# Kernel optimization log

Measured on AMD Instinct MI355X. Metric: run time of the kernel, lower is better.

Reference implementation:

```python
import jax, jax.numpy as jnp
import numpy as np
from jax import lax

B, L = 16384, 32
HID, CIN = 8, 2
N_SUB = 2            # RK4 substeps per spline interval (fixed-step stand-in for torchcde's adaptive solver)
T10_LO, T10_HI = 0.1, 7.0


def push_zeros(a):
    # torch: move nonzero entries of each row to the right end, zeros to the left.
    # stable ascending sort on validity key (0 for zeros, 1 for valid) reproduces this exactly
    # because the invalid entries are exactly 0.
    keys = (a != 0).astype(jnp.int32)
    order = jnp.argsort(keys, axis=1)  # jax sorts are stable
    return jnp.take_along_axis(a, order, axis=1)


def setup_inputs() -> dict:
    key = jax.random.key(0)
    ks = jax.random.split(key, 12)
    fa_len = jax.random.randint(ks[0], (B, 1), L // 2, L + 1)          # 16..32 valid points
    valid = jnp.arange(L)[None, :] < fa_len                             # (B, L)
    X_fa_in = jnp.where(valid, jax.random.uniform(ks[1], (B, L), minval=0.1, maxval=1.1), 0.0)
    fa_vals_in = jnp.where(valid, jax.random.uniform(ks[2], (B, L), minval=0.05, maxval=0.45), 0.0)
    TR_vals = jax.random.uniform(ks[3], (B, 1), minval=0.003, maxval=0.01)
    fa_mask = valid

    def lin(k, fout, fin):
        kw, kb = jax.random.split(k)
        s = 1.0 / np.sqrt(fin)
        return (jax.random.uniform(kw, (fout, fin), minval=-s, maxval=s),
                jax.random.uniform(kb, (fout,), minval=-s, maxval=s))

    W_init, b_init = lin(ks[4], HID, CIN)        # self.initial: Linear(2, 8)
    W1, b1 = lin(ks[5], 256, HID)                # CDE_Func.linear1
    W2, b2 = lin(ks[6], CIN * HID, 256)          # CDE_Func.linear2
    Wr1, br1 = lin(ks[7], 200, HID)              # reg_T10
    Wr2, br2 = lin(ks[8], 200, 200)
    Wr3, br3 = lin(ks[9], 1, 200)
    return dict(X_fa_in=X_fa_in, fa_vals_in=fa_vals_in, TR_vals=TR_vals,
                W_init=W_init, b_init=b_init, W1=W1, b1=b1, W2=W2, b2=b2,
                Wr1=Wr1, br1=br1, Wr2=Wr2, br2=br2, Wr3=Wr3, br3=br3,
                fa_mask=fa_mask, fa_len=fa_len)


def _forward(X_fa_in, fa_vals_in, TR_vals, W_init, b_init, W1, b1, W2, b2,
             Wr1, br1, Wr2, br2, Wr3, br3, fa_mask, fa_len):
    fl = fa_len[:, 0]                       # (B,) int
    fl_f = fl.astype(X_fa_in.dtype)
    mean = jnp.sum(X_fa_in, axis=1) / fl_f
    Xn = X_fa_in / mean[:, None]
    X_fa = push_zeros(Xn)
    fa_vals = push_zeros(fa_vals_in)
    bidx = jnp.arange(X_fa.shape[0])
    last_X = X_fa[bidx, fl - 1][:, None]            # pushed array indexed at fa_len-1 (as in torch)
    last_fa = fa_vals_in[bidx, fl - 1][:, None]     # original array indexed at fa_len-1
    X_fa = jnp.where(X_fa == 0.0, last_X, X_fa)
    fa_vals = jnp.where(fa_vals == 0.0, last_fa, fa_vals)
    x = jnp.stack([fa_vals, X_fa], axis=-1)         # (B, L, 2): channels (fa, X)

    # Hermite cubic with backward differences, unit knot spacing t_i = i
    diffs = x[:, 1:] - x[:, :-1]                    # (B, L-1, C)
    m = jnp.concatenate([diffs[:, :1], diffs], axis=1)  # m_0 = fwd diff, m_i = backward diff
    X0s, X1s = x[:, :-1], x[:, 1:]                  # per-interval knot values (B, L-1, C)
    M0s, M1s = m[:, :-1], m[:, 1:]

    z0 = x[:, 0] @ W_init.T + b_init                # X.evaluate(interval[0]) == first knot

    def f(z):  # CDE vector field: (B, HID) -> (B, HID, CIN)
        h = jax.nn.relu(z @ W1.T + b1)
        g = jnp.tanh(h @ W2.T + b2)
        return g.reshape(z.shape[0], HID, CIN)

    hstep = 1.0 / N_SUB
    nI = x.shape[1] - 1
    intervals = jnp.repeat(jnp.arange(nI), N_SUB)
    s0s = jnp.tile(jnp.arange(N_SUB) * hstep, nI).astype(x.dtype)

    def step(z, ts):
        i, s0 = ts
        x0, x1 = X0s[:, i], X1s[:, i]
        m0, m1 = M0s[:, i], M1s[:, i]

        def dX(s):  # spline derivative dX/dt at local coord s in [0,1]
            s2 = s * s
            return ((6 * s2 - 6 * s) * x0 + (3 * s2 - 4 * s + 1) * m0 +
                    (-6 * s2 + 6 * s) * x1 + (3 * s2 - 2 * s) * m1)

        def F(s, zz):
            return jnp.einsum('bhc,bc->bh', f(zz), dX(s))

        k1 = F(s0, z)
        k2 = F(s0 + hstep / 2, z + 0.5 * hstep * k1)
        k3 = F(s0 + hstep / 2, z + 0.5 * hstep * k2)
        k4 = F(s0 + hstep, z + hstep * k3)
        return z + (hstep / 6) * (k1 + 2 * k2 + 2 * k3 + k4), None

    z_T, _ = lax.scan(step, z0, (intervals, s0s))

    h1 = jax.nn.gelu(z_T @ Wr1.T + br1, approximate=False)
    h2 = jax.nn.gelu(h1 @ Wr2.T + br2, approximate=False)
    t = (h2 @ Wr3.T + br3)[:, 0]
    T10 = T10_LO + jax.nn.sigmoid(t)[:, None] * (T10_HI - T10_LO)   # (B, 1)
    R1 = 1.0 / T10
    E = jnp.exp(-TR_vals * R1)                                      # (B, 1)
    X_out = (1 - E) * jnp.sin(fa_vals_in) / (1 - jnp.cos(fa_vals_in) * E)
    mean2 = jnp.sum(X_out, axis=1) / fl_f
    X_out = X_out / mean2[:, None]
    M0 = jnp.ones_like(T10)
    return X_out, T10, M0


def reference(X_fa_in, fa_vals_in, TR_vals, W_init, b_init, W1, b1, W2, b2,
              Wr1, br1, Wr2, br2, Wr3, br3, fa_mask, fa_len):
    return _forward(X_fa_in, fa_vals_in, TR_vals, W_init, b_init, W1, b1, W2, b2,
                    Wr1, br1, Wr2, br2, Wr3, br3, fa_mask, fa_len)
```

## Files before the change

### kernel.cpp

```cpp
#include <hip/hip_runtime.h>
#include <hip/hip_bf16.h>

#define B_ROWS 16384
#define L_SEQ  32

typedef _Float16 f16;
typedef __attribute__((ext_vector_type(8))) _Float16 f16x8;
typedef __attribute__((ext_vector_type(4))) float f32x4;
typedef __attribute__((ext_vector_type(4))) unsigned int u32x4;

__device__ __forceinline__ unsigned pkh(float a, float b) {
    return __builtin_bit_cast(unsigned, __builtin_amdgcn_cvt_pkrtz(a, b));
}
__device__ __forceinline__ float tanh_fast(float x) {
    float e = __expf(2.0f * x);
    float r = __builtin_amdgcn_rcpf(e + 1.0f);
    return fmaf(-2.0f, r, 1.0f);
}
__device__ __forceinline__ float gelu_exact(float x) {
    return 0.5f * x * (1.0f + erff(x * 0.70710678118654752440f));
}
__device__ __forceinline__ void pin4(u32x4& v) {
    unsigned x0 = v[0], x1 = v[1], x2 = v[2], x3 = v[3];
    asm volatile("" : "+v"(x0), "+v"(x1), "+v"(x2), "+v"(x3));
    v = (u32x4){x0, x1, x2, x3};
}

__global__ __launch_bounds__(256, 1) void ode_kernel(
    const float* __restrict__ Xin, const float* __restrict__ Fin,
    const int*   __restrict__ fa_len,
    const float* __restrict__ Wi,  const float* __restrict__ bi,
    const float* __restrict__ W1g, const float* __restrict__ b1g,
    const float* __restrict__ W2g, const float* __restrict__ b2g,
    float* __restrict__ zT)
{
    __shared__ __align__(16) float xm[64 * 132];
#define XM(r_, i_, c_) xm[(r_) * 132 + (i_) * 4 + (c_)]

    const int tid = threadIdx.x;
    const int g16 = tid >> 4, sub = tid & 15;

    float mean_r[4]; int fl_r[4];
#pragma unroll
    for (int r = 0; r < 4; ++r) {
        const int row_l = g16 * 4 + r;
        const int row   = blockIdx.x * 64 + row_l;
        const float* Xr = Xin + row * L_SEQ;
        const float* Fr = Fin + row * L_SEQ;
        float xr0 = Xr[sub], xr1 = Xr[sub + 16];
        float fr0 = Fr[sub], fr1 = Fr[sub + 16];
        fl_r[r] = fa_len[row];
        float s = xr0 + xr1;
        s += __shfl_xor(s, 1, 16);
        s += __shfl_xor(s, 2, 16);
        s += __shfl_xor(s, 4, 16);
        s += __shfl_xor(s, 8, 16);
        mean_r[r] = s / (float)fl_r[r];
        XM(row_l, sub, 0)      = fr0; XM(row_l, sub, 1)      = xr0;
        XM(row_l, sub + 16, 0) = fr1; XM(row_l, sub + 16, 1) = xr1;
    }
    __syncthreads();

    float ff[4][2], xf[4][2];
#pragma unroll
    for (int r = 0; r < 4; ++r) {
        const int row_l = g16 * 4 + r;
        const int fl = fl_r[r];
        const float mean = mean_r[r];
        const int shift = L_SEQ - fl;
        int lsrc  = fl - 1 - shift;
        int lsrcC = lsrc < 0 ? 0 : lsrc;
        float lastX = (lsrc >= 0) ? (XM(row_l, lsrcC, 1) / mean) : 0.0f;
        float lastF = XM(row_l, fl - 1, 0);
#pragma unroll
        for (int u = 0; u < 2; ++u) {
            int p = sub + u * 16;
            int src = p - shift;
            int sc  = src < 0 ? 0 : src;
            float fraw = XM(row_l, sc, 0);
            float xraw = XM(row_l, sc, 1);
            ff[r][u] = (src >= 0) ? fraw : lastF;
            xf[r][u] = (src >= 0) ? (xraw / mean) : lastX;
        }
    }
    __syncthreads();
#pragma unroll
    for (int r = 0; r < 4; ++r) {
        const int row_l = g16 * 4 + r;
#pragma unroll
        for (int u = 0; u < 2; ++u) {
            int p = sub + u * 16;
            XM(row_l, p, 0) = ff[r][u];
            XM(row_l, p, 1) = xf[r][u];
        }
    }
    __syncthreads();
#pragma unroll
    for (int r = 0; r < 4; ++r) {
        const int row_l = g16 * 4 + r;
#pragma unroll
        for (int u = 0; u < 2; ++u) {
            int p = sub + u * 16;
            int qd = (p == 0) ? 1 : p;
            XM(row_l, p, 2) = XM(row_l, qd, 0) - XM(row_l, qd - 1, 0);
            XM(row_l, p, 3) = XM(row_l, qd, 1) - XM(row_l, qd - 1, 1);
        }
    }
    __syncthreads();

    const int wv   = tid >> 6;
    const int lane = tid & 63;
    const int n    = lane & 15;
    const int q    = lane >> 4;
    const int rowl = wv * 16 + n;
    const int rowg = blockIdx.x * 64 + rowl;

    u32x4 a1[16];
#pragma unroll
    for (int t = 0; t < 16; ++t) {
        const float* wr = W1g + (t * 16 + n) * 8 + (q < 2 ? q * 4 : 0);
        float4 w4 = *(const float4*)wr;
        float b1v = b1g[t * 16 + n];
        unsigned d0 = (q < 2) ? pkh(w4.x, w4.y) : (q == 2 ? pkh(b1v, 0.0f) : 0u);
        unsigned d1 = (q < 2) ? pkh(w4.z, w4.w) : 0u;
        a1[t] = (u32x4){d0, d1, 0u, 0u};
        pin4(a1[t]);
    }
    u32x4 a2[8];
#pragma unroll
    for (int kk = 0; kk < 8; ++kk) {
        const float* w2r = W2g + n * 256 + kk * 32 + 4 * q;
        float4 p0 = *(const float4*)(w2r);
        float4 p1 = *(const float4*)(w2r + 16);
        a2[kk] = (u32x4){pkh(p0.x, p0.y), pkh(p0.z, p0.w), pkh(p1.x, p1.y), pkh(p1.z, p1.w)};
        pin4(a2[kk]);
    }
    f32x4 c2seed;
#pragma unroll
    for (int r = 0; r < 4; ++r) c2seed[r] = b2g[4 * q + r];

    float f0 = XM(rowl, 0, 0), X0 = XM(rowl, 0, 1);
    float z0 = fmaf(Wi[(2 * q) * 2], f0, fmaf(Wi[(2 * q) * 2 + 1], X0, bi[2 * q]));
    float z1 = fmaf(Wi[(2 * q + 1) * 2], f0, fmaf(Wi[(2 * q + 1) * 2 + 1], X0, bi[2 * q + 1]));

    const int bpi = (((q & 1) << 5) + n) << 2;
    const f32x4 zero4 = {0.f, 0.f, 0.f, 0.f};
    const f16x8 zf16 = {0, 0, 0, 0, 0, 0, 0, 0};

    auto FEVAL = [&](float zza, float zzb, float d0c, float d1c, float& ko0, float& ko1) {
        unsigned myz = pkh(zza, zzb);
        int b0 = __builtin_amdgcn_ds_bpermute(bpi, (int)myz);
        int b1 = __builtin_amdgcn_ds_bpermute(bpi + 64, (int)myz);
        unsigned bz0 = (q < 2) ? (unsigned)b0 : (q == 2 ? 0x3C00u : 0u);
        unsigned bz1 = (q < 2) ? (unsigned)b1 : 0u;
        f16x8 bz = __builtin_bit_cast(f16x8, (u32x4){bz0, bz1, 0u, 0u});

        f32x4 c1[16];
#pragma unroll
        for (int t = 0; t < 16; ++t)
            c1[t] = __builtin_amdgcn_mfma_f32_16x16x32_f16(
                __builtin_bit_cast(f16x8, a1[t]), bz, zero4, 0, 0, 0);

        f16x8 hf[8];
#pragma unroll
        for (int kk = 0; kk < 8; ++kk) {
            u32x4 w = (u32x4){pkh(c1[2 * kk][0],     c1[2 * kk][1]),
                              pkh(c1[2 * kk][2],     c1[2 * kk][3]),
                              pkh(c1[2 * kk + 1][0], c1[2 * kk + 1][1]),
                              pkh(c1[2 * kk + 1][2], c1[2 * kk + 1][3])};
            hf[kk] = __builtin_elementwise_max(__builtin_bit_cast(f16x8, w), zf16);
        }

        f32x4 c2a = c2seed, c2b = zero4;
#pragma unroll
        for (int kk = 0; kk < 4; ++kk) {
            c2a = __builtin_amdgcn_mfma_f32_16x16x32_f16(
                __builtin_bit_cast(f16x8, a2[kk]), hf[kk], c2a, 0, 0, 0);
            c2b = __builtin_amdgcn_mfma_f32_16x16x32_f16(
                __builtin_bit_cast(f16x8, a2[kk + 4]), hf[kk + 4], c2b, 0, 0, 0);
        }
        f32x4 G = c2a + c2b;

        float t0 = tanh_fast(G[0]), t1 = tanh_fast(G[1]);
        float t2 = tanh_fast(G[2]), t3 = tanh_fast(G[3]);
        ko0 = fmaf(t0, d0c, t1 * d1c);
        ko1 = fmaf(t2, d0c, t3 * d1c);
    };

#pragma unroll 1
    for (int i = 0; i < 31; ++i) {
        float4 P0 = *(const float4*)&XM(rowl, i, 0);
        float4 P1 = *(const float4*)&XM(rowl, i + 1, 0);
        float m0f = P0.z, m0X = P0.w, m1f = P1.z, m1X = P1.w;
        float df  = P0.x - P1.x, dXx = P0.y - P1.y;

        float d25f = fmaf(-1.125f, df,  fmaf(0.1875f, m0f, -0.3125f * m1f));
        float d25X = fmaf(-1.125f, dXx, fmaf(0.1875f, m0X, -0.3125f * m1X));
        float d50f = fmaf(-1.5f,   df,  fmaf(-0.25f,  m0f, -0.25f   * m1f));
        float d50X = fmaf(-1.5f,   dXx, fmaf(-0.25f,  m0X, -0.25f   * m1X));
        float d75f = fmaf(-1.125f, df,  fmaf(-0.3125f, m0f, 0.1875f * m1f));
        float d75X = fmaf(-1.125f, dXx, fmaf(-0.3125f, m0X, 0.1875f * m1X));

#pragma unroll 1
        for (int ssi = 0; ssi < 2; ++ssi) {
            float daf = ssi ? d50f : m0f,  daX = ssi ? d50X : m0X;
            float dbf = ssi ? d75f : d25f, dbX = ssi ? d75X : d25X;
            float ddf = ssi ? m1f  : d50f, ddX = ssi ? m1X  : d50X;

            float k1a, k1b, k2a, k2b, k3a, k3b, k4a, k4b, zza, zzb;
            FEVAL(z0, z1, daf, daX, k1a, k1b);
            zza = fmaf(0.25f, k1a, z0); zzb = fmaf(0.25f, k1b, z1);
            FEVAL(zza, zzb, dbf, dbX, k2a, k2b);
            zza = fmaf(0.25f, k2a, z0); zzb = fmaf(0.25f, k2b, z1);
            FEVAL(zza, zzb, dbf, dbX, k3a, k3b);
            zza = fmaf(0.5f, k3a, z0);  zzb = fmaf(0.5f, k3b, z1);
            FEVAL(zza, zzb, ddf, ddX, k4a, k4b);

            float ka = fmaf(2.f, k2a, k1a); ka = fmaf(2.f, k3a, ka);
            float kb = fmaf(2.f, k2b, k1b); kb = fmaf(2.f, k3b, kb);
            z0 = fmaf(1.f / 12.f, ka + k4a, z0);
            z1 = fmaf(1.f / 12.f, kb + k4b, z1);
        }
    }

    *(float2*)(zT + rowg * 8 + 2 * q) = make_float2(z0, z1);
#undef XM
}

__global__ __launch_bounds__(256, 1) void readout_kernel(
    const float* __restrict__ zT,
    const float* __restrict__ Fin,
    const float* __restrict__ TRv,
    const int*   __restrict__ fa_len,
    const float* __restrict__ Wr1, const float* __restrict__ br1,
    const float* __restrict__ Wr2, const float* __restrict__ br2,
    const float* __restrict__ Wr3, const float* __restrict__ br3,
    float* __restrict__ out)
{
    const int tid  = threadIdx.x;
    const int wv   = tid >> 6;
    const int lane = tid & 63;
    const int n    = lane & 15;
    const int q    = lane >> 4;
    const int rowg = blockIdx.x * 64 + wv * 16 + n;

    const f32x4 zero4 = {0.f, 0.f, 0.f, 0.f};

    u32x4 bzw = {0u, 0u, 0u, 0u};
    if (q < 2) {
        float4 z4 = *(const float4*)(zT + rowg * 8 + 4 * q);
        bzw[0] = pkh(z4.x, z4.y);
        bzw[1] = pkh(z4.z, z4.w);
    } else if (q == 2) {
        bzw[0] = 0x3C00u;
    }
    f16x8 bz = __builtin_bit_cast(f16x8, bzw);

    f32x4 c1[13];
#pragma unroll
    for (int t = 0; t < 13; ++t) {
        int m = 16 * t + n;
        u32x4 af = {0u, 0u, 0u, 0u};
        if (q < 2) {
            if (m < 200) {
                float4 w4 = *(const float4*)(Wr1 + m * 8 + 4 * q);
                af[0] = pkh(w4.x, w4.y);
                af[1] = pkh(w4.z, w4.w);
            }
        } else if (q == 2) {
            float b = (m < 200) ? br1[m] : 0.0f;
            af[0] = pkh(b, 0.0f);
        }
        c1[t] = __builtin_amdgcn_mfma_f32_16x16x32_f16(
            __builtin_bit_cast(f16x8, af), bz, zero4, 0, 0, 0);
    }

    f16x8 hf[7];
#pragma unroll
    for (int kk = 0; kk < 7; ++kk) {
        float g0 = gelu_exact(c1[2 * kk][0]), g1 = gelu_exact(c1[2 * kk][1]);
        float g2 = gelu_exact(c1[2 * kk][2]), g3 = gelu_exact(c1[2 * kk][3]);
        float g4 = 0.f, g5 = 0.f, g6 = 0.f, g7 = 0.f;
        if (kk < 6) {
            g4 = gelu_exact(c1[2 * kk + 1][0]); g5 = gelu_exact(c1[2 * kk + 1][1]);
            g6 = gelu_exact(c1[2 * kk + 1][2]); g7 = gelu_exact(c1[2 * kk + 1][3]);
        }
        u32x4 w = (u32x4){pkh(g0, g1), pkh(g2, g3), pkh(g4, g5), pkh(g6, g7)};
        hf[kk] = __builtin_bit_cast(f16x8, w);
    }

    float tpart = 0.0f;
#pragma unroll 1
    for (int mt = 0; mt < 13; ++mt) {
        int mb = 16 * mt + 4 * q;
        f32x4 c2 = zero4;
        if (mb + 3 < 200) c2 = *(const f32x4*)(br2 + mb);
        int m2 = 16 * mt + n;
#pragma unroll
        for (int kk = 0; kk < 7; ++kk) {
            u32x4 af = {0u, 0u, 0u, 0u};
            if (m2 < 200) {
                int k0 = 32 * kk + 4 * q;
                const float* wr = Wr2 + m2 * 200 + k0;
                if (k0 + 3 < 200) {
                    float4 wa = *(const float4*)(wr);
                    af[0] = pkh(wa.x, wa.y); af[1] = pkh(wa.z, wa.w);
                }
                if (k0 + 19 < 200) {
                    float4 wb = *(const float4*)(wr + 16);
                    af[2] = pkh(wb.x, wb.y); af[3] = pkh(wb.z, wb.w);
                }
            }
            c2 = __builtin_amdgcn_mfma_f32_16x16x32_f16(
                __builtin_bit_cast(f16x8, af), hf[kk], c2, 0, 0, 0);
        }
        float4 w3 = make_float4(0.f, 0.f, 0.f, 0.f);
        if (mb + 3 < 200) w3 = *(const float4*)(Wr3 + mb);
        tpart = fmaf(w3.x, gelu_exact(c2[0]), tpart);
        tpart = fmaf(w3.y, gelu_exact(c2[1]), tpart);
        tpart = fmaf(w3.z, gelu_exact(c2[2]), tpart);
        tpart = fmaf(w3.w, gelu_exact(c2[3]), tpart);
    }
    tpart += __shfl_xor(tpart, 16);
    tpart += __shfl_xor(tpart, 32);

    float tval = tpart + br3[0];
    float sig  = __fdividef(1.0f, 1.0f + __expf(-tval));
    float T10  = 0.1f + 6.9f * sig;
    float E    = __expf(-TRv[rowg] * __builtin_amdgcn_rcpf(T10));

    const float* Fr = Fin + rowg * 32 + 8 * q;
    float xo[8]; float ssum = 0.0f;
#pragma unroll
    for (int j = 0; j < 8; ++j) {
        float fa = Fr[j];
        float sn = __sinf(fa), cs = __cosf(fa);
        float v = __fdividef((1.0f - E) * sn, 1.0f - cs * E);
        xo[j] = v; ssum += v;
    }
    ssum += __shfl_xor(ssum, 16);
    ssum += __shfl_xor(ssum, 32);
    float mean2 = ssum / (float)fa_len[rowg];
    float inv   = __fdividef(1.0f, mean2);

    float4* dst = (float4*)(out + rowg * 32 + 8 * q);
    dst[0] = make_float4(xo[0] * inv, xo[1] * inv, xo[2] * inv, xo[3] * inv);
    dst[1] = make_float4(xo[4] * inv, xo[5] * inv, xo[6] * inv, xo[7] * inv);
    if (q == 0) {
        out[B_ROWS * L_SEQ + rowg] = T10;
        out[B_ROWS * L_SEQ + B_ROWS + rowg] = 1.0f;
    }
}

extern "C" void kernel_launch(void* const* d_in, const int* in_sizes, int n_in,
                              void* d_out, int out_size, void* d_ws, size_t ws_size,
                              hipStream_t stream) {
    const float* Xin  = (const float*)d_in[0];
    const float* Fin  = (const float*)d_in[1];
    const float* TRv  = (const float*)d_in[2];
    const float* Wi   = (const float*)d_in[3];
    const float* bi   = (const float*)d_in[4];
    const float* W1g  = (const float*)d_in[5];
    const float* b1g  = (const float*)d_in[6];
    const float* W2g  = (const float*)d_in[7];
    const float* b2g  = (const float*)d_in[8];
    const float* Wr1  = (const float*)d_in[9];
    const float* br1  = (const float*)d_in[10];
    const float* Wr2  = (const float*)d_in[11];
    const float* br2  = (const float*)d_in[12];
    const float* Wr3  = (const float*)d_in[13];
    const float* br3  = (const float*)d_in[14];
    const int*   flen = (const int*)d_in[16];

    float* outp = (float*)d_out;
    float* zT   = (float*)d_ws;

    ode_kernel<<<dim3(B_ROWS / 64), dim3(256), 0, stream>>>(
        Xin, Fin, flen, Wi, bi, W1g, b1g, W2g, b2g, zT);
    readout_kernel<<<dim3(B_ROWS / 64), dim3(256), 0, stream>>>(
        zT, Fin, TRv, flen, Wr1, br1, Wr2, br2, Wr3, br3, outp);
}
```

Baseline: 273.5 us.

## Fuse ODE and readout kernels and stage Wr2 as fp16 in LDS

Merges the ODE-integration kernel and the regression-head readout kernel into one launch. The final hidden state is fed straight into the readout MFMAs through the same bpermute operand builder, so the zT workspace round trip and the second launch go away. Each block also converts Wr2 to fp16 once into a padded LDS tile, so the per-tile global loads and conversions of Wr2 in the readout loop become LDS reads. The price is roughly 96 KB of extra LDS per block and a prologue in every block that reads and converts the full Wr2 matrix, which limits blocks per CU.

```diff
diff --git a/kernel.cpp b/kernel.cpp
--- a/kernel.cpp
+++ b/kernel.cpp
@@ -26,19 +26,42 @@
     v = (u32x4){x0, x1, x2, x3};
 }
 
-__global__ __launch_bounds__(256, 1) void ode_kernel(
+#define W2S_STRIDE 232
+__global__ __launch_bounds__(256, 1) void fused_kernel(
     const float* __restrict__ Xin, const float* __restrict__ Fin,
+    const float* __restrict__ TRv,
     const int*   __restrict__ fa_len,
     const float* __restrict__ Wi,  const float* __restrict__ bi,
     const float* __restrict__ W1g, const float* __restrict__ b1g,
     const float* __restrict__ W2g, const float* __restrict__ b2g,
-    float* __restrict__ zT)
+    const float* __restrict__ Wr1, const float* __restrict__ br1,
+    const float* __restrict__ Wr2, const float* __restrict__ br2,
+    const float* __restrict__ Wr3, const float* __restrict__ br3,
+    float* __restrict__ out)
 {
     __shared__ __align__(16) float xm[64 * 132];
+    __shared__ __align__(16) unsigned short w2s[208 * W2S_STRIDE];
 #define XM(r_, i_, c_) xm[(r_) * 132 + (i_) * 4 + (c_)]
 
     const int tid = threadIdx.x;
     const int g16 = tid >> 4, sub = tid & 15;
+
+    {
+        const float4* src = (const float4*)Wr2;
+#pragma unroll 4
+        for (int v = tid; v < 10000; v += 256) {
+            int row = v / 50, c = (v - row * 50) * 4;
+            float4 w = src[v];
+            *(uint2*)(&w2s[row * W2S_STRIDE + c]) =
+                make_uint2(pkh(w.x, w.y), pkh(w.z, w.w));
+        }
+        for (int idx = tid; idx < 8 * W2S_STRIDE; idx += 256)
+            w2s[200 * W2S_STRIDE + idx] = 0;
+        for (int idx = tid; idx < 200 * 24; idx += 256) {
+            int row = idx / 24, c = 200 + (idx - row * 24);
+            w2s[row * W2S_STRIDE + c] = 0;
+        }
+    }
 
     float mean_r[4]; int fl_r[4];
 #pragma unroll
@@ -147,13 +170,17 @@
     const f32x4 zero4 = {0.f, 0.f, 0.f, 0.f};
     const f16x8 zf16 = {0, 0, 0, 0, 0, 0, 0, 0};
 
-    auto FEVAL = [&](float zza, float zzb, float d0c, float d1c, float& ko0, float& ko1) {
+    auto make_bz = [&](float zza, float zzb) -> f16x8 {
         unsigned myz = pkh(zza, zzb);
         int b0 = __builtin_amdgcn_ds_bpermute(bpi, (int)myz);
         int b1 = __builtin_amdgcn_ds_bpermute(bpi + 64, (int)myz);
         unsigned bz0 = (q < 2) ? (unsigned)b0 : (q == 2 ? 0x3C00u : 0u);
         unsigned bz1 = (q < 2) ? (unsigned)b1 : 0u;
-        f16x8 bz = __builtin_bit_cast(f16x8, (u32x4){bz0, bz1, 0u, 0u});
+        return __builtin_bit_cast(f16x8, (u32x4){bz0, bz1, 0u, 0u});
+    };
+
+    auto FEVAL = [&](float zza, float zzb, float d0c, float d1c, float& ko0, float& ko1) {
+        f16x8 bz = make_bz(zza, zzb);
 
         f32x4 c1[16];
 #pragma unroll
@@ -223,40 +250,8 @@
         }
     }
 
-    *(float2*)(zT + rowg * 8 + 2 * q) = make_float2(z0, z1);
-#undef XM
-}
-
-__global__ __launch_bounds__(256, 1) void readout_kernel(
-    const float* __restrict__ zT,
-    const float* __restrict__ Fin,
-    const float* __restrict__ TRv,
-    const int*   __restrict__ fa_len,
-    const float* __restrict__ Wr1, const float* __restrict__ br1,
-    const float* __restrict__ Wr2, const float* __restrict__ br2,
-    const float* __restrict__ Wr3, const float* __restrict__ br3,
-    float* __restrict__ out)
-{
-    const int tid  = threadIdx.x;
-    const int wv   = tid >> 6;
-    const int lane = tid & 63;
-    const int n    = lane & 15;
-    const int q    = lane >> 4;
-    const int rowg = blockIdx.x * 64 + wv * 16 + n;
-
-    const f32x4 zero4 = {0.f, 0.f, 0.f, 0.f};
-
-    u32x4 bzw = {0u, 0u, 0u, 0u};
-    if (q < 2) {
-        float4 z4 = *(const float4*)(zT + rowg * 8 + 4 * q);
-        bzw[0] = pkh(z4.x, z4.y);
-        bzw[1] = pkh(z4.z, z4.w);
-    } else if (q == 2) {
-        bzw[0] = 0x3C00u;
-    }
-    f16x8 bz = __builtin_bit_cast(f16x8, bzw);
-
-    f32x4 c1[13];
+    f16x8 bz = make_bz(z0, z1);
+    f32x4 c1r[13];
 #pragma unroll
     for (int t = 0; t < 13; ++t) {
         int m = 16 * t + n;
@@ -271,22 +266,22 @@
             float b = (m < 200) ? br1[m] : 0.0f;
             af[0] = pkh(b, 0.0f);
         }
-        c1[t] = __builtin_amdgcn_mfma_f32_16x16x32_f16(
+        c1r[t] = __builtin_amdgcn_mfma_f32_16x16x32_f16(
             __builtin_bit_cast(f16x8, af), bz, zero4, 0, 0, 0);
     }
 
-    f16x8 hf[7];
+    f16x8 hf2[7];
 #pragma unroll
     for (int kk = 0; kk < 7; ++kk) {
-        float g0 = gelu_exact(c1[2 * kk][0]), g1 = gelu_exact(c1[2 * kk][1]);
-        float g2 = gelu_exact(c1[2 * kk][2]), g3 = gelu_exact(c1[2 * kk][3]);
+        float g0 = gelu_exact(c1r[2 * kk][0]), g1 = gelu_exact(c1r[2 * kk][1]);
+        float g2 = gelu_exact(c1r[2 * kk][2]), g3 = gelu_exact(c1r[2 * kk][3]);
         float g4 = 0.f, g5 = 0.f, g6 = 0.f, g7 = 0.f;
         if (kk < 6) {
-            g4 = gelu_exact(c1[2 * kk + 1][0]); g5 = gelu_exact(c1[2 * kk + 1][1]);
-            g6 = gelu_exact(c1[2 * kk + 1][2]); g7 = gelu_exact(c1[2 * kk + 1][3]);
+            g4 = gelu_exact(c1r[2 * kk + 1][0]); g5 = gelu_exact(c1r[2 * kk + 1][1]);
+            g6 = gelu_exact(c1r[2 * kk + 1][2]); g7 = gelu_exact(c1r[2 * kk + 1][3]);
         }
         u32x4 w = (u32x4){pkh(g0, g1), pkh(g2, g3), pkh(g4, g5), pkh(g6, g7)};
-        hf[kk] = __builtin_bit_cast(f16x8, w);
+        hf2[kk] = __builtin_bit_cast(f16x8, w);
     }
 
     float tpart = 0.0f;
@@ -295,24 +290,14 @@
         int mb = 16 * mt + 4 * q;
         f32x4 c2 = zero4;
         if (mb + 3 < 200) c2 = *(const f32x4*)(br2 + mb);
-        int m2 = 16 * mt + n;
+        const unsigned short* ap = &w2s[(16 * mt + n) * W2S_STRIDE + 4 * q];
 #pragma unroll
         for (int kk = 0; kk < 7; ++kk) {
-            u32x4 af = {0u, 0u, 0u, 0u};
-            if (m2 < 200) {
-                int k0 = 32 * kk + 4 * q;
-                const float* wr = Wr2 + m2 * 200 + k0;
-                if (k0 + 3 < 200) {
-                    float4 wa = *(const float4*)(wr);
-                    af[0] = pkh(wa.x, wa.y); af[1] = pkh(wa.z, wa.w);
-                }
-                if (k0 + 19 < 200) {
-                    float4 wb = *(const float4*)(wr + 16);
-                    af[2] = pkh(wb.x, wb.y); af[3] = pkh(wb.z, wb.w);
-                }
-            }
+            uint2 lo = *(const uint2*)(ap + 32 * kk);
+            uint2 hi = *(const uint2*)(ap + 32 * kk + 16);
+            u32x4 af = {lo.x, lo.y, hi.x, hi.y};
             c2 = __builtin_amdgcn_mfma_f32_16x16x32_f16(
-                __builtin_bit_cast(f16x8, af), hf[kk], c2, 0, 0, 0);
+                __builtin_bit_cast(f16x8, af), hf2[kk], c2, 0, 0, 0);
         }
         float4 w3 = make_float4(0.f, 0.f, 0.f, 0.f);
         if (mb + 3 < 200) w3 = *(const float4*)(Wr3 + mb);
@@ -350,6 +335,7 @@
         out[B_ROWS * L_SEQ + rowg] = T10;
         out[B_ROWS * L_SEQ + B_ROWS + rowg] = 1.0f;
     }
+#undef XM
 }
 
 extern "C" void kernel_launch(void* const* d_in, const int* in_sizes, int n_in,
@@ -373,10 +359,9 @@
     const int*   flen = (const int*)d_in[16];
 
     float* outp = (float*)d_out;
-    float* zT   = (float*)d_ws;
-
-    ode_kernel<<<dim3(B_ROWS / 64), dim3(256), 0, stream>>>(
-        Xin, Fin, flen, Wi, bi, W1g, b1g, W2g, b2g, zT);
-    readout_kernel<<<dim3(B_ROWS / 64), dim3(256), 0, stream>>>(
-        zT, Fin, TRv, flen, Wr1, br1, Wr2, br2, Wr3, br3, outp);
-}
+    (void)d_ws; (void)ws_size;
+
+    fused_kernel<<<dim3(B_ROWS / 64), dim3(256), 0, stream>>>(
+        Xin, Fin, TRv, flen, Wi, bi, W1g, b1g, W2g, b2g,
+        Wr1, br1, Wr2, br2, Wr3, br3, outp);
+}
```

New measurement: 251.7 us. -8.0%, faster.
